# Performance work log

Measured on AMD Instinct MI355X. Metric: run time of the kernel, lower is better.

The kernel has to match this reference:

```python
import jax, jax.numpy as jnp
import numpy as np

K = 128      # classes
CIN = 128    # ch_in
CL = 128     # ch_latent
B, H, W = 8, 1, 8192
SLOPE = 0.01 # F.leaky_relu default
EPS = 1e-5   # BatchNorm eps


def lrelu(x):
    return jnp.where(x >= 0, x, SLOPE * x)


def conv1x1(x, w, b):
    # x: (B,C,H,W), w: (O,C), b: (O,)
    return jnp.einsum('bchw,oc->bohw', x, w) + b[None, :, None, None]


def bn_eval(x, gamma, beta, mean, var):
    scale = gamma * jax.lax.rsqrt(var + EPS)
    return x * scale[None, :, None, None] + (beta - mean * scale)[None, :, None, None]


def setup_inputs() -> dict:
    key = jax.random.key(0)
    ks = jax.random.split(key, 16)
    def w(k, shape, fan_in):
        return jax.random.normal(k, shape, jnp.float32) / np.sqrt(fan_in)
    return {
        'x_in': jax.random.normal(ks[0], (B, CIN, H, W), jnp.float32),
        'cl1_w': w(ks[1], (CL, CIN), CIN), 'cl1_b': jnp.zeros((CL,), jnp.float32),
        'bn1_gamma': jnp.ones((CL,), jnp.float32), 'bn1_beta': jnp.zeros((CL,), jnp.float32),
        'bn1_mean': 0.1 * jax.random.normal(ks[2], (CL,), jnp.float32),
        'bn1_var': jax.random.uniform(ks[3], (CL,), jnp.float32, 0.5, 1.5),
        'cl2_w': w(ks[4], (CL, CL), CL), 'cl2_b': jnp.zeros((CL,), jnp.float32),
        'cl3_w': w(ks[5], (K + 1, CL), CL), 'cl3_b': jnp.zeros((K + 1,), jnp.float32),
        'reg1_w': w(ks[6], (CL, CIN), CIN), 'reg1_b': jnp.zeros((CL,), jnp.float32),
        'bnr_gamma': jnp.ones((CL,), jnp.float32), 'bnr_beta': jnp.zeros((CL,), jnp.float32),
        'bnr_mean': 0.1 * jax.random.normal(ks[7], (CL,), jnp.float32),
        'bnr_var': jax.random.uniform(ks[8], (CL,), jnp.float32, 0.5, 1.5),
        'cm2_w': w(ks[9], (K, CL, 32), CL), 'cm2_b': jnp.zeros((K, 32), jnp.float32),
        'cm3_w': w(ks[10], (K, 32, 1), 32), 'cm3_b': jnp.zeros((K, 1), jnp.float32),
    }


def reference(x_in, cl1_w, cl1_b, bn1_gamma, bn1_beta, bn1_mean, bn1_var,
              cl2_w, cl2_b, cl3_w, cl3_b,
              reg1_w, reg1_b, bnr_gamma, bnr_beta, bnr_mean, bnr_var,
              cm2_w, cm2_b, cm3_w, cm3_b):
    # classification branch
    x = lrelu(bn_eval(conv1x1(x_in, cl1_w, cl1_b), bn1_gamma, bn1_beta, bn1_mean, bn1_var))
    x = lrelu(conv1x1(x, cl2_w, cl2_b))
    x = conv1x1(x, cl3_w, cl3_b)                    # (B, K+1, H, W)
    logits = x[:, :K]
    mask = lrelu(x[:, -1:])                          # (B,1,H,W)
    inds = jnp.argmax(logits, axis=1)                # (B,H,W) int
    inds_r = inds.reshape(-1).astype(jnp.int32)      # (N,)
    xr = lrelu(bn_eval(conv1x1(x_in, reg1_w, reg1_b), bnr_gamma, bnr_beta, bnr_mean, bnr_var))
    # torch: transpose(1,3).reshape(-1, C)  -> (B,W,H,C) flatten
    xr = jnp.transpose(xr, (0, 3, 2, 1)).reshape(-1, CL)   # (N, CL)
    # CondMul 1: per-pixel gathered weight (N,CL,32)
    h = lrelu(jnp.einsum('ni,nio->no', xr, cm2_w[inds_r]) + cm2_b[inds_r])
    # CondMul 2: (N,32)->(N,1)
    reg = jnp.einsum('ni,nio->no', h, cm3_w[inds_r]) + cm3_b[inds_r]
    reg = reg.reshape(B, 1, 1, -1)                   # (B,1,1,H*W)
    x_real = (inds[:, None].astype(jnp.float32) + reg) * (1.0 / K)
    return x_real, mask
```

## Files before the change

kernel.cpp:

```cpp
#include <hip/hip_runtime.h>
#include <math.h>

#define NPOS 65536
#define NCH  128
#define DELTA 0.008f
#define HPAD 16

#define OFF_XR   0u
#define OFF_W1T  8388608u
#define OFF_W2T  (OFF_W1T + 16384u)
#define OFF_W3T  (OFF_W2T + 16384u)
#define OFF_B1F  (OFF_W3T + 16384u)
#define OFF_BRF  (OFF_B1F + 128u)
#define OFF_B2F  (OFF_BRF + 128u)
#define OFF_B3F  (OFF_B2F + 128u)
#define OFF_BF16 (OFF_B3F + 132u)
#define OFF_INT  (OFF_BF16 + 329728u)

#define UW1H 0u
#define UW1L 16384u
#define UWRH 32768u
#define UWRL 49152u
#define UW2H 65536u
#define UW2L 81920u
#define UW3H 98304u
#define UW3L 116736u
#define UW2K 135168u

#define NST 2080

typedef short bf16x8 __attribute__((ext_vector_type(8)));
typedef float f32x4 __attribute__((ext_vector_type(4)));
#define MFMA16 __builtin_amdgcn_mfma_f32_16x16x32_bf16

__device__ __forceinline__ float lrelu(float v) { return v >= 0.0f ? v : 0.01f * v; }
__device__ __forceinline__ unsigned short f2bf(float f) {
    unsigned u = __float_as_uint(f);
    return (unsigned short)((u + 0x7fffu + ((u >> 16) & 1u)) >> 16);
}
__device__ __forceinline__ float bf2f(unsigned short h) {
    return __uint_as_float(((unsigned)h) << 16);
}
__device__ __forceinline__ unsigned long long pack4(unsigned short a, unsigned short b,
                                                    unsigned short c, unsigned short d) {
    return (unsigned long long)a | ((unsigned long long)b << 16)
         | ((unsigned long long)c << 32) | ((unsigned long long)d << 48);
}

__global__ void k_prep(const float* __restrict__ cl1_w, const float* __restrict__ cl1_b,
                       const float* __restrict__ g1, const float* __restrict__ be1,
                       const float* __restrict__ mu1, const float* __restrict__ va1,
                       const float* __restrict__ cl2_w, const float* __restrict__ cl2_b,
                       const float* __restrict__ cl3_w, const float* __restrict__ cl3_b,
                       const float* __restrict__ reg1_w, const float* __restrict__ reg1_b,
                       const float* __restrict__ gr, const float* __restrict__ ber,
                       const float* __restrict__ mur, const float* __restrict__ var_,
                       const float* __restrict__ cm2w,
                       float* __restrict__ ws_f, unsigned short* __restrict__ wbf,
                       int* __restrict__ hist, int* __restrict__ cur)
{
    const int bid = blockIdx.x;
    const int t = threadIdx.x;
    if (bid >= 128) {
        __shared__ float tl[32 * 132];
        int k = bid - 128;
        #pragma unroll
        for (int i = 0; i < 32; ++i) {
            float v = cm2w[(unsigned)k * 4096u + i * 128 + t];
            int ci = i * 4 + (t >> 5), o = t & 31;
            tl[o * 132 + ci] = v;
        }
        __syncthreads();
        #pragma unroll
        for (int i = 0; i < 32; ++i)
            wbf[UW2K + (unsigned)k * 4096u + i * 128 + t] = f2bf(tl[i * 132 + t]);
        return;
    }
    const int cout = bid;
    const int cin = t;
    const int row = cout * 128 + cin;
    float s1 = g1[cout] / sqrtf(va1[cout] + 1e-5f);
    float sr = gr[cout] / sqrtf(var_[cout] + 1e-5f);
    float w1 = cl1_w[row] * s1;
    float wr = reg1_w[row] * sr;
    float w2 = cl2_w[row];
    float w3 = cl3_w[row];
    ws_f[OFF_W1T + cin * 128 + cout] = w1;
    ws_f[OFF_W2T + cin * 128 + cout] = w2;
    ws_f[OFF_W3T + cin * 128 + cout] = w3;
    unsigned short h;
    h = f2bf(w1); wbf[UW1H + row] = h; wbf[UW1L + row] = f2bf(w1 - bf2f(h));
    h = f2bf(wr); wbf[UWRH + row] = h; wbf[UWRL + row] = f2bf(wr - bf2f(h));
    h = f2bf(w2); wbf[UW2H + row] = h; wbf[UW2L + row] = f2bf(w2 - bf2f(h));
    h = f2bf(w3); wbf[UW3H + row] = h; wbf[UW3L + row] = f2bf(w3 - bf2f(h));
    if (bid < 16) {
        float v = (bid == 0) ? cl3_w[128 * 128 + t] : 0.0f;
        int jj = (128 + bid) * 128 + t;
        h = f2bf(v); wbf[UW3H + jj] = h; wbf[UW3L + jj] = f2bf(v - bf2f(h));
    }
    if (bid == 0) {
        float s1b = g1[t] / sqrtf(va1[t] + 1e-5f);
        float srb = gr[t] / sqrtf(var_[t] + 1e-5f);
        ws_f[OFF_B1F + t] = cl1_b[t] * s1b + be1[t] - mu1[t] * s1b;
        ws_f[OFF_BRF + t] = reg1_b[t] * srb + ber[t] - mur[t] * srb;
        ws_f[OFF_B2F + t] = cl2_b[t];
        ws_f[OFF_B3F + t] = cl3_b[t];
        hist[t * HPAD] = 0;
        cur[t * HPAD] = 0;
    }
    if (bid == 1 && t == 0) ws_f[OFF_B3F + 128] = cl3_b[128];
}

__global__ __launch_bounds__(256, 4)
void k_fused(const float* __restrict__ X, const float* __restrict__ wsf,
             const unsigned short* __restrict__ wbf,
             unsigned short* __restrict__ XRB, float* __restrict__ out_mask,
             int* __restrict__ inds, int* __restrict__ hist)
{
    __shared__ __align__(16) unsigned short XBh[64 * 136];
    __shared__ __align__(16) unsigned short XBl[64 * 136];
    __shared__ float sm1[4 * 64];
    __shared__ float sm2[4 * 64];
    __shared__ int   si1[4 * 64];
    __shared__ int   locid[64];
    __shared__ int   flist[64];
    __shared__ int   fcntS;
    __shared__ int   lh[128];

    const int t = threadIdx.x;
    const int lane = t & 63;
    const int cl16 = lane & 15;
    const int q8 = (lane >> 4) * 8;
    const int q4 = (lane >> 4) * 4;
    const int wv = __builtin_amdgcn_readfirstlane(t >> 6);
    const unsigned nt64 = blockIdx.x * 64u;
    const unsigned base = nt64 + (nt64 >> 13) * 1040384u;

    const unsigned short* W1H = wbf + UW1H; const unsigned short* W1L = wbf + UW1L;
    const unsigned short* WRH = wbf + UWRH; const unsigned short* WRL = wbf + UWRL;
    const unsigned short* W2H = wbf + UW2H; const unsigned short* W2L = wbf + UW2L;
    const unsigned short* W3H = wbf + UW3H; const unsigned short* W3L = wbf + UW3L;
    const float* b1f = wsf + OFF_B1F;
    const float* brf = wsf + OFF_BRF;
    const float* b2f = wsf + OFF_B2F;
    const float* b3f = wsf + OFF_B3F;

    const f32x4 vzero = {0.f, 0.f, 0.f, 0.f};

    if (t == 0) fcntS = 0;

    {
        const int pos = t & 63, cig = t >> 6;
        #pragma unroll
        for (int l = 0; l < 8; ++l) {
            int ci0 = cig * 32 + l * 4;
            float v0 = X[base + (unsigned)(ci0 + 0) * 8192u + pos];
            float v1 = X[base + (unsigned)(ci0 + 1) * 8192u + pos];
            float v2 = X[base + (unsigned)(ci0 + 2) * 8192u + pos];
            float v3 = X[base + (unsigned)(ci0 + 3) * 8192u + pos];
            unsigned short h0 = f2bf(v0), h1 = f2bf(v1), h2 = f2bf(v2), h3 = f2bf(v3);
            unsigned long long ph = pack4(h0, h1, h2, h3);
            unsigned long long pl = pack4(f2bf(v0 - bf2f(h0)), f2bf(v1 - bf2f(h1)),
                                          f2bf(v2 - bf2f(h2)), f2bf(v3 - bf2f(h3)));
            *(unsigned long long*)&XBh[pos * 136 + ci0] = ph;
            *(unsigned long long*)&XBl[pos * 136 + ci0] = pl;
        }
    }
    __syncthreads();

    f32x4 acc[2][4];

    #pragma unroll
    for (int m = 0; m < 2; ++m)
        #pragma unroll
        for (int n = 0; n < 4; ++n) acc[m][n] = vzero;
    #pragma unroll
    for (int kt = 0; kt < 4; ++kt) {
        bf16x8 Bh[4], Bl[4];
        #pragma unroll
        for (int n = 0; n < 4; ++n) {
            int bo = (n * 16 + cl16) * 136 + kt * 32 + q8;
            Bh[n] = *(const bf16x8*)&XBh[bo];
            Bl[n] = *(const bf16x8*)&XBl[bo];
        }
        #pragma unroll
        for (int m = 0; m < 2; ++m) {
            int ao = (wv * 32 + m * 16 + cl16) * 128 + kt * 32 + q8;
            bf16x8 arh = *(const bf16x8*)&WRH[ao], arl = *(const bf16x8*)&WRL[ao];
            #pragma unroll
            for (int n = 0; n < 4; ++n) {
                acc[m][n] = MFMA16(arh, Bl[n], acc[m][n], 0, 0, 0);
                acc[m][n] = MFMA16(arl, Bh[n], acc[m][n], 0, 0, 0);
                acc[m][n] = MFMA16(arh, Bh[n], acc[m][n], 0, 0, 0);
            }
        }
    }
    {
        #pragma unroll
        for (int m = 0; m < 2; ++m) {
            int cb = wv * 32 + m * 16 + q4;
            float br0 = brf[cb], br1 = brf[cb + 1], br2 = brf[cb + 2], br3 = brf[cb + 3];
            #pragma unroll
            for (int n = 0; n < 4; ++n) {
                unsigned pb = (nt64 + n * 16 + cl16) * 128u + cb;
                ushort4 xo;
                xo.x = f2bf(lrelu(acc[m][n][0] + br0));
                xo.y = f2bf(lrelu(acc[m][n][1] + br1));
                xo.z = f2bf(lrelu(acc[m][n][2] + br2));
                xo.w = f2bf(lrelu(acc[m][n][3] + br3));
                *(ushort4*)&XRB[pb] = xo;
            }
        }
    }

    #pragma unroll
    for (int m = 0; m < 2; ++m)
        #pragma unroll
        for (int n = 0; n < 4; ++n) acc[m][n] = vzero;
    #pragma unroll
    for (int kt = 0; kt < 4; ++kt) {
        bf16x8 Bh[4], Bl[4];
        #pragma unroll
        for (int n = 0; n < 4; ++n) {
            int bo = (n * 16 + cl16) * 136 + kt * 32 + q8;
            Bh[n] = *(const bf16x8*)&XBh[bo];
            Bl[n] = *(const bf16x8*)&XBl[bo];
        }
        #pragma unroll
        for (int m = 0; m < 2; ++m) {
            int ao = (wv * 32 + m * 16 + cl16) * 128 + kt * 32 + q8;
            bf16x8 a1h = *(const bf16x8*)&W1H[ao], a1l = *(const bf16x8*)&W1L[ao];
            #pragma unroll
            for (int n = 0; n < 4; ++n) {
                acc[m][n] = MFMA16(a1h, Bl[n], acc[m][n], 0, 0, 0);
                acc[m][n] = MFMA16(a1l, Bh[n], acc[m][n], 0, 0, 0);
                acc[m][n] = MFMA16(a1h, Bh[n], acc[m][n], 0, 0, 0);
            }
        }
    }
    __syncthreads();
    {
        #pragma unroll
        for (int m = 0; m < 2; ++m) {
            int cb = wv * 32 + m * 16 + q4;
            float b0 = b1f[cb], b1 = b1f[cb + 1], b2 = b1f[cb + 2], b3 = b1f[cb + 3];
            #pragma unroll
            for (int n = 0; n < 4; ++n) {
                float v0 = lrelu(acc[m][n][0] + b0), v1 = lrelu(acc[m][n][1] + b1);
                float v2 = lrelu(acc[m][n][2] + b2), v3 = lrelu(acc[m][n][3] + b3);
                unsigned short h0 = f2bf(v0), h1 = f2bf(v1), h2 = f2bf(v2), h3 = f2bf(v3);
                unsigned long long ph = pack4(h0, h1, h2, h3);
                unsigned long long pl = pack4(f2bf(v0 - bf2f(h0)), f2bf(v1 - bf2f(h1)),
                                              f2bf(v2 - bf2f(h2)), f2bf(v3 - bf2f(h3)));
                int idx = (n * 16 + cl16) * 136 + cb;
                *(unsigned long long*)&XBh[idx] = ph;
                *(unsigned long long*)&XBl[idx] = pl;
            }
        }
    }
    __syncthreads();

    #pragma unroll
    for (int m = 0; m < 2; ++m)
        #pragma unroll
        for (int n = 0; n < 4; ++n) acc[m][n] = vzero;
    #pragma unroll
    for (int kt = 0; kt < 4; ++kt) {
        bf16x8 Bh[4], Bl[4];
        #pragma unroll
        for (int n = 0; n < 4; ++n) {
            int bo = (n * 16 + cl16) * 136 + kt * 32 + q8;
            Bh[n] = *(const bf16x8*)&XBh[bo];
            Bl[n] = *(const bf16x8*)&XBl[bo];
        }
        #pragma unroll
        for (int m = 0; m < 2; ++m) {
            int ao = (wv * 32 + m * 16 + cl16) * 128 + kt * 32 + q8;
            bf16x8 ah = *(const bf16x8*)&W2H[ao], al = *(const bf16x8*)&W2L[ao];
            #pragma unroll
            for (int n = 0; n < 4; ++n) {
                acc[m][n] = MFMA16(ah, Bl[n], acc[m][n], 0, 0, 0);
                acc[m][n] = MFMA16(al, Bh[n], acc[m][n], 0, 0, 0);
                acc[m][n] = MFMA16(ah, Bh[n], acc[m][n], 0, 0, 0);
            }
        }
    }
    __syncthreads();
    {
        #pragma unroll
        for (int m = 0; m < 2; ++m) {
            int cb = wv * 32 + m * 16 + q4;
            float b0 = b2f[cb], b1 = b2f[cb + 1], b2 = b2f[cb + 2], b3 = b2f[cb + 3];
            #pragma unroll
            for (int n = 0; n < 4; ++n) {
                float v0 = lrelu(acc[m][n][0] + b0), v1 = lrelu(acc[m][n][1] + b1);
                float v2 = lrelu(acc[m][n][2] + b2), v3 = lrelu(acc[m][n][3] + b3);
                unsigned short h0 = f2bf(v0), h1 = f2bf(v1), h2 = f2bf(v2), h3 = f2bf(v3);
                unsigned long long ph = pack4(h0, h1, h2, h3);
                unsigned long long pl = pack4(f2bf(v0 - bf2f(h0)), f2bf(v1 - bf2f(h1)),
                                              f2bf(v2 - bf2f(h2)), f2bf(v3 - bf2f(h3)));
                int idx = (n * 16 + cl16) * 136 + cb;
                *(unsigned long long*)&XBh[idx] = ph;
                *(unsigned long long*)&XBl[idx] = pl;
            }
        }
    }
    __syncthreads();

    f32x4 accM = vzero;
    #pragma unroll
    for (int m = 0; m < 2; ++m)
        #pragma unroll
        for (int n = 0; n < 4; ++n) acc[m][n] = vzero;
    #pragma unroll
    for (int kt = 0; kt < 4; ++kt) {
        bf16x8 Bh[4], Bl[4];
        #pragma unroll
        for (int n = 0; n < 4; ++n) {
            int bo = (n * 16 + cl16) * 136 + kt * 32 + q8;
            Bh[n] = *(const bf16x8*)&XBh[bo];
            Bl[n] = *(const bf16x8*)&XBl[bo];
        }
        #pragma unroll
        for (int m = 0; m < 2; ++m) {
            int ao = (wv * 32 + m * 16 + cl16) * 128 + kt * 32 + q8;
            bf16x8 ah = *(const bf16x8*)&W3H[ao], al = *(const bf16x8*)&W3L[ao];
            #pragma unroll
            for (int n = 0; n < 4; ++n) {
                acc[m][n] = MFMA16(ah, Bl[n], acc[m][n], 0, 0, 0);
                acc[m][n] = MFMA16(al, Bh[n], acc[m][n], 0, 0, 0);
                acc[m][n] = MFMA16(ah, Bh[n], acc[m][n], 0, 0, 0);
            }
        }
        {
            int boM = (wv * 16 + cl16) * 136 + kt * 32 + q8;
            bf16x8 BhM = *(const bf16x8*)&XBh[boM];
            bf16x8 BlM = *(const bf16x8*)&XBl[boM];
            int ao = (128 + cl16) * 128 + kt * 32 + q8;
            bf16x8 ah = *(const bf16x8*)&W3H[ao], al = *(const bf16x8*)&W3L[ao];
            accM = MFMA16(ah, BlM, accM, 0, 0, 0);
            accM = MFMA16(al, BhM, accM, 0, 0, 0);
            accM = MFMA16(ah, BhM, accM, 0, 0, 0);
        }
    }

    {
        float bb[2][4];
        #pragma unroll
        for (int m = 0; m < 2; ++m) {
            int cb = wv * 32 + m * 16 + q4;
            bb[m][0] = b3f[cb]; bb[m][1] = b3f[cb + 1];
            bb[m][2] = b3f[cb + 2]; bb[m][3] = b3f[cb + 3];
        }
        float m1[4], m2[4]; int i1[4];
        #pragma unroll
        for (int n = 0; n < 4; ++n) {
            m1[n] = -1e30f; m2[n] = -1e30f; i1[n] = 0;
            #pragma unroll
            for (int m = 0; m < 2; ++m) {
                int cb = wv * 32 + m * 16 + q4;
                #pragma unroll
                for (int r = 0; r < 4; ++r) {
                    float v = acc[m][n][r] + bb[m][r];
                    if (v > m1[n]) { m2[n] = m1[n]; m1[n] = v; i1[n] = cb + r; }
                    else if (v > m2[n]) m2[n] = v;
                }
            }
        }
        #pragma unroll
        for (int off = 16; off <= 32; off <<= 1) {
            #pragma unroll
            for (int n = 0; n < 4; ++n) {
                float om1 = __shfl_xor(m1[n], off);
                float om2 = __shfl_xor(m2[n], off);
                int   oi1 = __shfl_xor(i1[n], off);
                if (om1 > m1[n] || (om1 == m1[n] && oi1 < i1[n])) {
                    m2[n] = fmaxf(m1[n], om2); m1[n] = om1; i1[n] = oi1;
                } else {
                    m2[n] = fmaxf(m2[n], om1);
                }
            }
        }
        if ((lane >> 4) == 0) {
            #pragma unroll
            for (int n = 0; n < 4; ++n) {
                sm1[wv * 64 + n * 16 + cl16] = m1[n];
                sm2[wv * 64 + n * 16 + cl16] = m2[n];
                si1[wv * 64 + n * 16 + cl16] = i1[n];
            }
        }
    }
    if ((lane >> 4) == 0) {
        float mb = b3f[128];
        out_mask[nt64 + wv * 16 + cl16] = lrelu(accM[0] + mb);
    }
    __syncthreads();
    if (t < 64) {
        float m1 = sm1[t], m2 = sm2[t];
        int i1 = si1[t];
        #pragma unroll
        for (int w = 1; w < 4; ++w) {
            float v1 = sm1[w * 64 + t];
            float v2 = sm2[w * 64 + t];
            int   vi = si1[w * 64 + t];
            if (v1 > m1) { m2 = fmaxf(m1, v2); m1 = v1; i1 = vi; }
            else         { m2 = fmaxf(m2, v1); }
        }
        int n = nt64 + t;
        inds[n] = i1;
        locid[t] = i1;
        if (m1 - m2 < DELTA) {
            int slot = atomicAdd(&fcntS, 1);
            flist[slot] = t;
        }
    }
    __syncthreads();

    {
        const int fc = fcntS;
        const float* W1T = wsf + OFF_W1T;
        const float* W2T = wsf + OFF_W2T;
        const float* W3T = wsf + OFF_W3T;
        for (int i = wv; i < fc; i += 4) {
            int pos = flist[i];
            int n = nt64 + pos;
            const float* xb = X + (unsigned)(n >> 13) * 1048576u + (unsigned)(n & 8191);
            float x0 = xb[(unsigned)lane * 8192u];
            float x1 = xb[(unsigned)(64 + lane) * 8192u];
            float a0, a1;
            a0 = 0.f; a1 = 0.f;
            for (int ci = 0; ci < 64; ++ci) {
                float xv = __shfl(x0, ci);
                const float* wr = W1T + ci * 128;
                a0 = fmaf(wr[lane], xv, a0);
                a1 = fmaf(wr[64 + lane], xv, a1);
            }
            for (int ci = 0; ci < 64; ++ci) {
                float xv = __shfl(x1, ci);
                const float* wr = W1T + (64 + ci) * 128;
                a0 = fmaf(wr[lane], xv, a0);
                a1 = fmaf(wr[64 + lane], xv, a1);
            }
            x0 = lrelu(a0 + b1f[lane]); x1 = lrelu(a1 + b1f[64 + lane]);
            a0 = 0.f; a1 = 0.f;
            for (int ci = 0; ci < 64; ++ci) {
                float xv = __shfl(x0, ci);
                const float* wr = W2T + ci * 128;
                a0 = fmaf(wr[lane], xv, a0);
                a1 = fmaf(wr[64 + lane], xv, a1);
            }
            for (int ci = 0; ci < 64; ++ci) {
                float xv = __shfl(x1, ci);
                const float* wr = W2T + (64 + ci) * 128;
                a0 = fmaf(wr[lane], xv, a0);
                a1 = fmaf(wr[64 + lane], xv, a1);
            }
            x0 = lrelu(a0 + b2f[lane]); x1 = lrelu(a1 + b2f[64 + lane]);
            a0 = 0.f; a1 = 0.f;
            for (int ci = 0; ci < 64; ++ci) {
                float xv = __shfl(x0, ci);
                const float* wr = W3T + ci * 128;
                a0 = fmaf(wr[lane], xv, a0);
                a1 = fmaf(wr[64 + lane], xv, a1);
            }
            for (int ci = 0; ci < 64; ++ci) {
                float xv = __shfl(x1, ci);
                const float* wr = W3T + (64 + ci) * 128;
                a0 = fmaf(wr[lane], xv, a0);
                a1 = fmaf(wr[64 + lane], xv, a1);
            }
            float L0 = a0 + b3f[lane], L1 = a1 + b3f[64 + lane];
            float v; int id;
            if (L0 >= L1) { v = L0; id = lane; } else { v = L1; id = 64 + lane; }
            #pragma unroll
            for (int off = 1; off < 64; off <<= 1) {
                float ov = __shfl_xor(v, off);
                int   oi = __shfl_xor(id, off);
                if (ov > v || (ov == v && oi < id)) { v = ov; id = oi; }
            }
            if (lane == 0) { inds[n] = id; locid[pos] = id; }
        }
    }
    __syncthreads();

    if (t < 128) lh[t] = 0;
    __syncthreads();
    if (t < 64) atomicAdd(&lh[locid[t]], 1);
    __syncthreads();
    if (t < 128 && lh[t] > 0) atomicAdd(&hist[t * HPAD], lh[t]);
}

__global__ void k_scatter(const int* __restrict__ inds, const int* __restrict__ hist,
                          int* __restrict__ cur, int* __restrict__ bucket)
{
    __shared__ int lh[128];
    __shared__ int gb[128];
    __shared__ int sv[128];
    __shared__ int sh[128];
    int t = threadIdx.x;
    if (t < 128) { int h = hist[t * HPAD]; sh[t] = h; sv[t] = h; lh[t] = 0; }
    __syncthreads();
    for (int d = 1; d < 128; d <<= 1) {
        int a = (t < 128 && t >= d) ? sv[t - d] : 0;
        __syncthreads();
        if (t < 128) sv[t] += a;
        __syncthreads();
    }
    int n = blockIdx.x * 256 + t;
    int id = inds[n];
    int r = atomicAdd(&lh[id], 1);
    __syncthreads();
    if (t < 128 && lh[t] > 0)
        gb[t] = (sv[t] - sh[t]) + atomicAdd(&cur[t * HPAD], lh[t]);
    __syncthreads();
    bucket[gb[id] + r] = n;
}

__global__ __launch_bounds__(256, 4)
void k_reg(const unsigned short* __restrict__ XRB, const unsigned short* __restrict__ wbf,
           const float* __restrict__ cm2b, const float* __restrict__ cm3w,
           const float* __restrict__ cm3b, const int* __restrict__ hist,
           const int* __restrict__ bucket, float* __restrict__ out)
{
    __shared__ __align__(16) unsigned short XP[4 * NST];
    __shared__ float red[64];
    __shared__ int sh[128];
    __shared__ int sv[128];
    __shared__ int st[128];
    __shared__ int skj[2];
    int bid = blockIdx.x;
    int t = threadIdx.x;
    if (t < 128) {
        int h = hist[t * HPAD];
        sh[t] = h; sv[t] = h; st[t] = (h + 63) >> 6;
    }
    __syncthreads();
    for (int d = 1; d < 128; d <<= 1) {
        int a = (t < 128 && t >= d) ? sv[t - d] : 0;
        int b = (t < 128 && t >= d) ? st[t - d] : 0;
        __syncthreads();
        if (t < 128) { sv[t] += a; st[t] += b; }
        __syncthreads();
    }
    if (bid >= st[127]) return;
    if (t < 128) {
        int ntk = (sh[t] + 63) >> 6;
        int tb = st[t] - ntk;
        if (bid >= tb && bid < st[t]) { skj[0] = t; skj[1] = bid - tb; }
    }
    __syncthreads();
    const int k = skj[0];
    const int start = skj[1] << 6;
    const int cnt = sh[k];
    const int base = sv[k] - sh[k];
    int lane = t & 63;
    int wv = __builtin_amdgcn_readfirstlane(t >> 6);
    const int n16 = lane & 15;
    const int quad = lane >> 4;

    {
        int rs = t >> 2;
        int q = t & 3;
        int sidx = start + rs;
        if (sidx >= cnt) sidx = cnt - 1;
        int n = bucket[base + sidx];
        const uint4* src = (const uint4*)(XRB + (unsigned)n * 128u + q * 32);
        uint4 a0 = src[0], a1 = src[1], a2 = src[2], a3 = src[3];
        unsigned db = (rs >> 4) * NST + q * 512 + (rs & 15) * 8;
        *(uint4*)&XP[db]       = a0;
        *(uint4*)&XP[db + 128] = a1;
        *(uint4*)&XP[db + 256] = a2;
        *(uint4*)&XP[db + 384] = a3;
    }
    __syncthreads();

    const unsigned short* wb = wbf + UW2K + (unsigned)k * 4096u;
    bf16x8 Bf[2][4];
    #pragma unroll
    for (int nf = 0; nf < 2; ++nf)
        #pragma unroll
        for (int kt = 0; kt < 4; ++kt)
            Bf[nf][kt] = *(const bf16x8*)&wb[(nf * 16 + n16) * 128 + kt * 32 + quad * 8];

    const f32x4 vzero = {0.f, 0.f, 0.f, 0.f};
    f32x4 acc[2];
    acc[0] = vzero; acc[1] = vzero;
    #pragma unroll
    for (int kt = 0; kt < 4; ++kt) {
        bf16x8 Af = *(const bf16x8*)&XP[wv * NST + kt * 512 + lane * 8];
        #pragma unroll
        for (int nf = 0; nf < 2; ++nf)
            acc[nf] = MFMA16(Af, Bf[nf][kt], acc[nf], 0, 0, 0);
    }

    float b2a = cm2b[k * 32 + n16], b2b = cm2b[k * 32 + 16 + n16];
    float w3a = cm3w[k * 32 + n16], w3b = cm3w[k * 32 + 16 + n16];
    #pragma unroll
    for (int r = 0; r < 4; ++r) {
        float p = lrelu(acc[0][r] + b2a) * w3a
                + lrelu(acc[1][r] + b2b) * w3b;
        p += __shfl_xor(p, 1);
        p += __shfl_xor(p, 2);
        p += __shfl_xor(p, 4);
        p += __shfl_xor(p, 8);
        if (n16 == 0)
            red[wv * 16 + quad * 4 + r] = p;
    }
    __syncthreads();
    if (t < 64 && start + t < cnt) {
        int n2 = bucket[base + start + t];
        out[n2] = ((float)k + red[t] + cm3b[k]) * (1.0f / 128.0f);
    }
}

extern "C" void kernel_launch(void* const* d_in, const int* in_sizes, int n_in,
                              void* d_out, int out_size, void* d_ws, size_t ws_size,
                              hipStream_t stream)
{
    (void)in_sizes; (void)n_in; (void)out_size; (void)ws_size;
    const float* x_in   = (const float*)d_in[0];
    const float* cl1_w  = (const float*)d_in[1];
    const float* cl1_b  = (const float*)d_in[2];
    const float* g1     = (const float*)d_in[3];
    const float* be1    = (const float*)d_in[4];
    const float* mu1    = (const float*)d_in[5];
    const float* va1    = (const float*)d_in[6];
    const float* cl2_w  = (const float*)d_in[7];
    const float* cl2_b  = (const float*)d_in[8];
    const float* cl3_w  = (const float*)d_in[9];
    const float* cl3_b  = (const float*)d_in[10];
    const float* reg1_w = (const float*)d_in[11];
    const float* reg1_b = (const float*)d_in[12];
    const float* gr     = (const float*)d_in[13];
    const float* ber    = (const float*)d_in[14];
    const float* mur    = (const float*)d_in[15];
    const float* var_   = (const float*)d_in[16];
    const float* cm2w   = (const float*)d_in[17];
    const float* cm2b   = (const float*)d_in[18];
    const float* cm3w   = (const float*)d_in[19];
    const float* cm3b   = (const float*)d_in[20];

    float* ws_f = (float*)d_ws;
    unsigned short* XRB = (unsigned short*)(ws_f + OFF_XR);
    unsigned short* wbf = (unsigned short*)(ws_f + OFF_BF16);
    int*   wsi    = (int*)(ws_f + OFF_INT);
    int*   inds   = wsi;
    int*   hist   = inds + 65536;
    int*   offb   = hist + 2048;
    int*   cur    = offb + 128;
    int*   ntt    = cur + 2048;
    int*   fixcnt = ntt + 4;
    int*   tiles  = fixcnt + 4;
    int*   fixlist= tiles + 1536;
    int*   bucket = fixlist + 65536;
    float* out = (float*)d_out;

    hipLaunchKernelGGL(k_prep, dim3(256), dim3(128), 0, stream,
                       cl1_w, cl1_b, g1, be1, mu1, va1, cl2_w, cl2_b, cl3_w, cl3_b,
                       reg1_w, reg1_b, gr, ber, mur, var_, cm2w, ws_f, wbf, hist, cur);
    hipLaunchKernelGGL(k_fused, dim3(1024), dim3(256), 0, stream,
                       x_in, ws_f, wbf, XRB, out + 65536, inds, hist);
    hipLaunchKernelGGL(k_scatter, dim3(256), dim3(256), 0, stream,
                       inds, hist, cur, bucket);
    hipLaunchKernelGGL(k_reg, dim3(1536), dim3(256), 0, stream,
                       XRB, wbf, cm2b, cm3w, cm3b, hist, bucket, out);
}
```

Before: 205.3 us.

## Move fp32 argmax fix-up of near-tie pixels into a separate balanced kernel

Near-tie pixels, whose top-two logits differ by less than a threshold, were previously recomputed in exact fp32 inside each fused block. That made blocks with many ties stragglers and held every block's resources longer. The change appends these pixels to a global list via an atomic counter, and a new k_fix kernel spreads the recompute evenly across all waves. It then corrects the global histogram with atomic subtract/add when the index changes. This costs an extra launch and global atomics on the tie list, but removes the per-block tail from the main fused kernel.

```diff
diff --git a/kernel.cpp b/kernel.cpp
--- a/kernel.cpp
+++ b/kernel.cpp
@@ -57,7 +57,8 @@
                        const float* __restrict__ mur, const float* __restrict__ var_,
                        const float* __restrict__ cm2w,
                        float* __restrict__ ws_f, unsigned short* __restrict__ wbf,
-                       int* __restrict__ hist, int* __restrict__ cur)
+                       int* __restrict__ hist, int* __restrict__ cur,
+                       int* __restrict__ fixcnt)
 {
     const int bid = blockIdx.x;
     const int t = threadIdx.x;
@@ -108,23 +109,21 @@
         hist[t * HPAD] = 0;
         cur[t * HPAD] = 0;
     }
-    if (bid == 1 && t == 0) ws_f[OFF_B3F + 128] = cl3_b[128];
+    if (bid == 1 && t == 0) { ws_f[OFF_B3F + 128] = cl3_b[128]; fixcnt[0] = 0; }
 }
 
 __global__ __launch_bounds__(256, 4)
 void k_fused(const float* __restrict__ X, const float* __restrict__ wsf,
              const unsigned short* __restrict__ wbf,
              unsigned short* __restrict__ XRB, float* __restrict__ out_mask,
-             int* __restrict__ inds, int* __restrict__ hist)
+             int* __restrict__ inds, int* __restrict__ hist,
+             int* __restrict__ fixcnt, int* __restrict__ fixlist)
 {
     __shared__ __align__(16) unsigned short XBh[64 * 136];
     __shared__ __align__(16) unsigned short XBl[64 * 136];
     __shared__ float sm1[4 * 64];
     __shared__ float sm2[4 * 64];
     __shared__ int   si1[4 * 64];
-    __shared__ int   locid[64];
-    __shared__ int   flist[64];
-    __shared__ int   fcntS;
     __shared__ int   lh[128];
 
     const int t = threadIdx.x;
@@ -146,8 +145,6 @@
     const float* b3f = wsf + OFF_B3F;
 
     const f32x4 vzero = {0.f, 0.f, 0.f, 0.f};
-
-    if (t == 0) fcntS = 0;
 
     {
         const int pos = t & 63, cig = t >> 6;
@@ -394,6 +391,7 @@
         float mb = b3f[128];
         out_mask[nt64 + wv * 16 + cl16] = lrelu(accM[0] + mb);
     }
+    if (t < 128) lh[t] = 0;
     __syncthreads();
     if (t < 64) {
         float m1 = sm1[t], m2 = sm2[t];
@@ -408,86 +406,95 @@
         }
         int n = nt64 + t;
         inds[n] = i1;
-        locid[t] = i1;
+        atomicAdd(&lh[i1], 1);
         if (m1 - m2 < DELTA) {
-            int slot = atomicAdd(&fcntS, 1);
-            flist[slot] = t;
-        }
-    }
-    __syncthreads();
-
-    {
-        const int fc = fcntS;
-        const float* W1T = wsf + OFF_W1T;
-        const float* W2T = wsf + OFF_W2T;
-        const float* W3T = wsf + OFF_W3T;
-        for (int i = wv; i < fc; i += 4) {
-            int pos = flist[i];
-            int n = nt64 + pos;
-            const float* xb = X + (unsigned)(n >> 13) * 1048576u + (unsigned)(n & 8191);
-            float x0 = xb[(unsigned)lane * 8192u];
-            float x1 = xb[(unsigned)(64 + lane) * 8192u];
-            float a0, a1;
-            a0 = 0.f; a1 = 0.f;
-            for (int ci = 0; ci < 64; ++ci) {
-                float xv = __shfl(x0, ci);
-                const float* wr = W1T + ci * 128;
-                a0 = fmaf(wr[lane], xv, a0);
-                a1 = fmaf(wr[64 + lane], xv, a1);
-            }
-            for (int ci = 0; ci < 64; ++ci) {
-                float xv = __shfl(x1, ci);
-                const float* wr = W1T + (64 + ci) * 128;
-                a0 = fmaf(wr[lane], xv, a0);
-                a1 = fmaf(wr[64 + lane], xv, a1);
-            }
-            x0 = lrelu(a0 + b1f[lane]); x1 = lrelu(a1 + b1f[64 + lane]);
-            a0 = 0.f; a1 = 0.f;
-            for (int ci = 0; ci < 64; ++ci) {
-                float xv = __shfl(x0, ci);
-                const float* wr = W2T + ci * 128;
-                a0 = fmaf(wr[lane], xv, a0);
-                a1 = fmaf(wr[64 + lane], xv, a1);
-            }
-            for (int ci = 0; ci < 64; ++ci) {
-                float xv = __shfl(x1, ci);
-                const float* wr = W2T + (64 + ci) * 128;
-                a0 = fmaf(wr[lane], xv, a0);
-                a1 = fmaf(wr[64 + lane], xv, a1);
-            }
-            x0 = lrelu(a0 + b2f[lane]); x1 = lrelu(a1 + b2f[64 + lane]);
-            a0 = 0.f; a1 = 0.f;
-            for (int ci = 0; ci < 64; ++ci) {
-                float xv = __shfl(x0, ci);
-                const float* wr = W3T + ci * 128;
-                a0 = fmaf(wr[lane], xv, a0);
-                a1 = fmaf(wr[64 + lane], xv, a1);
-            }
-            for (int ci = 0; ci < 64; ++ci) {
-                float xv = __shfl(x1, ci);
-                const float* wr = W3T + (64 + ci) * 128;
-                a0 = fmaf(wr[lane], xv, a0);
-                a1 = fmaf(wr[64 + lane], xv, a1);
-            }
-            float L0 = a0 + b3f[lane], L1 = a1 + b3f[64 + lane];
-            float v; int id;
-            if (L0 >= L1) { v = L0; id = lane; } else { v = L1; id = 64 + lane; }
-            #pragma unroll
-            for (int off = 1; off < 64; off <<= 1) {
-                float ov = __shfl_xor(v, off);
-                int   oi = __shfl_xor(id, off);
-                if (ov > v || (ov == v && oi < id)) { v = ov; id = oi; }
-            }
-            if (lane == 0) { inds[n] = id; locid[pos] = id; }
-        }
-    }
-    __syncthreads();
-
-    if (t < 128) lh[t] = 0;
-    __syncthreads();
-    if (t < 64) atomicAdd(&lh[locid[t]], 1);
+            int slot = atomicAdd(fixcnt, 1);
+            fixlist[slot] = n;
+        }
+    }
     __syncthreads();
     if (t < 128 && lh[t] > 0) atomicAdd(&hist[t * HPAD], lh[t]);
+}
+
+__global__ __launch_bounds__(256, 4)
+void k_fix(const float* __restrict__ X, const float* __restrict__ wsf,
+           const int* __restrict__ fixcnt, const int* __restrict__ fixlist,
+           int* __restrict__ inds, int* __restrict__ hist)
+{
+    const int cnt = fixcnt[0];
+    const int t = threadIdx.x;
+    const int lane = t & 63;
+    const int wv = t >> 6;
+    const float* W1T = wsf + OFF_W1T;
+    const float* W2T = wsf + OFF_W2T;
+    const float* W3T = wsf + OFF_W3T;
+    const float* b1f = wsf + OFF_B1F;
+    const float* b2f = wsf + OFF_B2F;
+    const float* b3f = wsf + OFF_B3F;
+
+    for (int idx = blockIdx.x * 4 + wv; idx < cnt; idx += 1024) {
+        int n = fixlist[idx];
+        int oldid = inds[n];
+        const float* xb = X + (unsigned)(n >> 13) * 1048576u + (unsigned)(n & 8191);
+        float x0 = xb[(unsigned)lane * 8192u];
+        float x1 = xb[(unsigned)(64 + lane) * 8192u];
+        float a0, a1;
+        a0 = 0.f; a1 = 0.f;
+        for (int ci = 0; ci < 64; ++ci) {
+            float xv = __shfl(x0, ci);
+            const float* wr = W1T + ci * 128;
+            a0 = fmaf(wr[lane], xv, a0);
+            a1 = fmaf(wr[64 + lane], xv, a1);
+        }
+        for (int ci = 0; ci < 64; ++ci) {
+            float xv = __shfl(x1, ci);
+            const float* wr = W1T + (64 + ci) * 128;
+            a0 = fmaf(wr[lane], xv, a0);
+            a1 = fmaf(wr[64 + lane], xv, a1);
+        }
+        x0 = lrelu(a0 + b1f[lane]); x1 = lrelu(a1 + b1f[64 + lane]);
+        a0 = 0.f; a1 = 0.f;
+        for (int ci = 0; ci < 64; ++ci) {
+            float xv = __shfl(x0, ci);
+            const float* wr = W2T + ci * 128;
+            a0 = fmaf(wr[lane], xv, a0);
+            a1 = fmaf(wr[64 + lane], xv, a1);
+        }
+        for (int ci = 0; ci < 64; ++ci) {
+            float xv = __shfl(x1, ci);
+            const float* wr = W2T + (64 + ci) * 128;
+            a0 = fmaf(wr[lane], xv, a0);
+            a1 = fmaf(wr[64 + lane], xv, a1);
+        }
+        x0 = lrelu(a0 + b2f[lane]); x1 = lrelu(a1 + b2f[64 + lane]);
+        a0 = 0.f; a1 = 0.f;
+        for (int ci = 0; ci < 64; ++ci) {
+            float xv = __shfl(x0, ci);
+            const float* wr = W3T + ci * 128;
+            a0 = fmaf(wr[lane], xv, a0);
+            a1 = fmaf(wr[64 + lane], xv, a1);
+        }
+        for (int ci = 0; ci < 64; ++ci) {
+            float xv = __shfl(x1, ci);
+            const float* wr = W3T + (64 + ci) * 128;
+            a0 = fmaf(wr[lane], xv, a0);
+            a1 = fmaf(wr[64 + lane], xv, a1);
+        }
+        float L0 = a0 + b3f[lane], L1 = a1 + b3f[64 + lane];
+        float v; int id;
+        if (L0 >= L1) { v = L0; id = lane; } else { v = L1; id = 64 + lane; }
+        #pragma unroll
+        for (int off = 1; off < 64; off <<= 1) {
+            float ov = __shfl_xor(v, off);
+            int   oi = __shfl_xor(id, off);
+            if (ov > v || (ov == v && oi < id)) { v = ov; id = oi; }
+        }
+        if (lane == 0 && id != oldid) {
+            inds[n] = id;
+            atomicSub(&hist[oldid * HPAD], 1);
+            atomicAdd(&hist[id * HPAD], 1);
+        }
+    }
 }
 
 __global__ void k_scatter(const int* __restrict__ inds, const int* __restrict__ hist,
@@ -657,9 +664,12 @@
 
     hipLaunchKernelGGL(k_prep, dim3(256), dim3(128), 0, stream,
                        cl1_w, cl1_b, g1, be1, mu1, va1, cl2_w, cl2_b, cl3_w, cl3_b,
-                       reg1_w, reg1_b, gr, ber, mur, var_, cm2w, ws_f, wbf, hist, cur);
+                       reg1_w, reg1_b, gr, ber, mur, var_, cm2w, ws_f, wbf, hist, cur,
+                       fixcnt);
     hipLaunchKernelGGL(k_fused, dim3(1024), dim3(256), 0, stream,
-                       x_in, ws_f, wbf, XRB, out + 65536, inds, hist);
+                       x_in, ws_f, wbf, XRB, out + 65536, inds, hist, fixcnt, fixlist);
+    hipLaunchKernelGGL(k_fix, dim3(256), dim3(256), 0, stream,
+                       x_in, ws_f, fixcnt, fixlist, inds, hist);
     hipLaunchKernelGGL(k_scatter, dim3(256), dim3(256), 0, stream,
                        inds, hist, cur, bucket);
     hipLaunchKernelGGL(k_reg, dim3(1536), dim3(256), 0, stream,
```

Result: slower. 219.4 us (+6.9%).
